# Performance work log

Measured on AMD Instinct MI355X. Metric: run time of the kernel, lower is better.

## Reference

```python
import jax, jax.numpy as jnp
import numpy as np

B, T, TREF, C, H = 2, 2048, 512, 768, 12
D = C // H


def setup_inputs() -> dict:
    key = jax.random.key(0)
    ks = jax.random.split(key, 20)
    s = 0.02  # init scale for weights
    inp = {
        "x": jax.random.normal(ks[0], (B, T, C), dtype=jnp.float32),
        "mask": jax.random.randint(ks[1], (B, 1, T, T), 0, 2, dtype=jnp.int32),
        "rel_pos": jax.random.normal(ks[2], (H, T, T), dtype=jnp.float32) * 0.1,
        "ref_feat": jax.random.normal(ks[3], (B, TREF, C), dtype=jnp.float32),
    }
    names = ["Wq", "Wk", "Wv", "Wrk", "Wrv", "Wo"]
    for i, n in enumerate(names):
        inp[n] = jax.random.normal(ks[4 + i], (C, C), dtype=jnp.float32) * s
        inp["b" + n[1:]] = jnp.zeros((C,), dtype=jnp.float32)
    return inp


def _heads(t, W, b):
    # nn.Linear: y = t @ W.T + b, then (B, L, H, D) -> (B, H, L, D)
    Bt, L, _ = t.shape
    return (t @ W.T + b).reshape(Bt, L, H, D).transpose(0, 2, 1, 3)


def reference(x, mask, rel_pos, ref_feat, Wq, bq, Wk, bk, Wv, bv,
              Wrk, brk, Wrv, brv, Wo, bo):
    Bx, Tx, Cx = x.shape
    Tref = ref_feat.shape[1]
    q = _heads(x, Wq, bq)                  # (B,H,T,D)
    k = _heads(x, Wk, bk)
    v = _heads(x, Wv, bv)
    rk = _heads(ref_feat, Wrk, brk)        # (B,H,Tref,D)
    rv = _heads(ref_feat, Wrv, brv)
    k = jnp.concatenate([k, rk], axis=2)   # (B,H,T+Tref,D)
    v = jnp.concatenate([v, rv], axis=2)
    # additive bias: -inf where mask==1 (self keys), rel_pos on self keys,
    # ref keys get 0 bias (mask padded with 0)
    bias_self = jnp.where(mask == 1, -jnp.inf, 0.0).astype(x.dtype) + rel_pos[None]  # (B,H,T,T)
    bias = jnp.pad(bias_self, ((0, 0), (0, 0), (0, 0), (0, Tref)))  # (B,H,T,T+Tref)
    scale = 1.0 / jnp.sqrt(jnp.asarray(D, dtype=x.dtype))
    scores = jnp.einsum('bhqd,bhkd->bhqk', q, k) * scale + bias
    attn = jax.nn.softmax(scores, axis=-1)
    y = jnp.einsum('bhqk,bhkd->bhqd', attn, v)
    y = y.transpose(0, 2, 1, 3).reshape(Bx, Tx, Cx)
    return y @ Wo.T + bo
```

## Files before the change

### kernel.cpp

```cpp
#include <hip/hip_runtime.h>


typedef __bf16 bf16x8 __attribute__((ext_vector_type(8)));
typedef float floatx4 __attribute__((ext_vector_type(4)));
typedef uint uintx2 __attribute__((ext_vector_type(2)));

__device__ __forceinline__ ushort f2bf(float f) {
  uint u = __builtin_bit_cast(uint, f);
  return (ushort)((u + 0x7FFFu + ((u >> 16) & 1u)) >> 16);
}

__device__ __forceinline__ uint pack2bf(float lo, float hi) {
  ushort a = __builtin_bit_cast(ushort, (__bf16)lo);
  ushort b = __builtin_bit_cast(ushort, (__bf16)hi);
  return (uint)a | ((uint)b << 16);
}

__device__ __forceinline__ float fexp2(float x) {
#if __has_builtin(__builtin_amdgcn_exp2f)
  return __builtin_amdgcn_exp2f(x);
#else
  return exp2f(x);
#endif
}

__device__ __forceinline__ void gld16(ushort* lds, const ushort* g) {
  __builtin_amdgcn_global_load_lds(
      (const __attribute__((address_space(1))) unsigned int*)g,
      (__attribute__((address_space(3))) unsigned int*)lds, 16, 0, 0);
}

__global__ __launch_bounds__(256) void cast_all(
    const float* __restrict__ x, const float* __restrict__ rf,
    const float* __restrict__ w0, const float* __restrict__ w1,
    const float* __restrict__ w2, const float* __restrict__ w3,
    const float* __restrict__ w4, const float* __restrict__ w5,
    ushort* __restrict__ dst) {
  size_t i4 = ((size_t)blockIdx.x * 256 + threadIdx.x) * 4;
  const float* src;
  size_t off;
  if (i4 < 3145728) { src = x; off = i4; }
  else if (i4 < 3932160) { src = rf; off = i4 - 3145728; }
  else {
    size_t r = i4 - 3932160;
    if (r < 589824) { src = w0; off = r; }
    else if (r < 2 * 589824) { src = w1; off = r - 589824; }
    else if (r < 3 * 589824) { src = w2; off = r - 2 * 589824; }
    else if (r < 4 * 589824) { src = w3; off = r - 3 * 589824; }
    else if (r < 5 * 589824) { src = w4; off = r - 4 * 589824; }
    else { src = w5; off = r - 5 * 589824; }
  }
  float4 v = *(const float4*)(src + off);
  ushort4 o;
  o.x = f2bf(v.x); o.y = f2bf(v.y); o.z = f2bf(v.z); o.w = f2bf(v.w);
  *(ushort4*)(dst + i4) = o;
}

__global__ __launch_bounds__(256) void pack_mask(
    const int* __restrict__ mask, unsigned long long* __restrict__ bits) {
  const int gid = blockIdx.x * 256 + threadIdx.x;
  const int4* src = (const int4*)(mask + (size_t)gid * 64);
  unsigned long long v = 0;
#pragma unroll
  for (int j = 0; j < 16; ++j) {
    int4 m = src[j];
    unsigned long long nib = (m.x ? 1ull : 0ull) | (m.y ? 2ull : 0ull) |
                             (m.z ? 4ull : 0ull) | (m.w ? 8ull : 0ull);
    v |= nib << (j * 4);
  }
  bits[gid] = v;
}

__device__ __forceinline__ void gemm_core(
    const ushort* __restrict__ Ab, const ushort* __restrict__ Bb,
    ushort* As, ushort* Bs, int tid, int quad, int l16, int mw, int nw,
    floatx4 acc[4][4]) {
  const int w = tid >> 6;
  const int r0 = tid >> 2, kp = (tid & 3) * 8;
  const size_t ga0 = (size_t)r0 * 768 + kp;
  const size_t ga1 = ga0 + (size_t)64 * 768;
#define GEMM_ISSUE(kb, p)                                   \
  do {                                                      \
    const int k0_ = (kb) * 32;                              \
    gld16(&As[(p) * 4096 + w * 512], Ab + ga0 + k0_);       \
    gld16(&As[(p) * 4096 + w * 512 + 2048], Ab + ga1 + k0_);\
    gld16(&Bs[(p) * 4096 + w * 512], Bb + ga0 + k0_);       \
    gld16(&Bs[(p) * 4096 + w * 512 + 2048], Bb + ga1 + k0_);\
  } while (0)
  GEMM_ISSUE(0, 0);
#pragma unroll 1
  for (int kb = 0; kb < 24; ++kb) {
    __syncthreads();
    if (kb < 23) GEMM_ISSUE(kb + 1, (kb + 1) & 1);
    const int p = kb & 1;
    bf16x8 af[4], bfr[4];
#pragma unroll
    for (int mt = 0; mt < 4; ++mt)
      af[mt] = *(const bf16x8*)&As[p * 4096 + (mw + mt * 16 + l16) * 32 + quad * 8];
#pragma unroll
    for (int nt = 0; nt < 4; ++nt)
      bfr[nt] = *(const bf16x8*)&Bs[p * 4096 + (nw + nt * 16 + l16) * 32 + quad * 8];
#pragma unroll
    for (int mt = 0; mt < 4; ++mt)
#pragma unroll
      for (int nt = 0; nt < 4; ++nt)
        acc[mt][nt] = __builtin_amdgcn_mfma_f32_16x16x32_bf16(af[mt], bfr[nt], acc[mt][nt], 0, 0, 0);
  }
#undef GEMM_ISSUE
}

template <int REF>
__global__ __launch_bounds__(256) void gemm_fused(
    const ushort* __restrict__ A, const ushort* __restrict__ W,
    const float* __restrict__ bA, const float* __restrict__ bB,
    const float* __restrict__ bC,
    ushort* __restrict__ oA, ushort* __restrict__ oB, ushort* __restrict__ oC) {
  const int bm = blockIdx.x, bn = blockIdx.y;
  const int tid = threadIdx.x;
  const int w = tid >> 6, lane = tid & 63, quad = lane >> 4, l16 = lane & 15;
  const int mw = (w >> 1) * 64, nw = (w & 1) * 64;

  __shared__ __align__(16) ushort As[2 * 4096];
  __shared__ __align__(16) ushort Bs[2 * 4096];

  floatx4 acc[4][4];
#pragma unroll
  for (int mt = 0; mt < 4; ++mt)
#pragma unroll
    for (int nt = 0; nt < 4; ++nt) acc[mt][nt] = (floatx4){0.f, 0.f, 0.f, 0.f};

  gemm_core(A + (size_t)bm * 128 * 768, W + (size_t)bn * 128 * 768,
            As, Bs, tid, quad, l16, mw, nw, acc);

  const int sec = bn / 6;
  const float* bp = sec == 0 ? bA : sec == 1 ? bB : bC;
  ushort* op = sec == 0 ? oA : sec == 1 ? oB : oC;
  const bool qlay = (REF == 0 && sec == 0);
  const bool vlay = (REF == 0) ? (sec == 2) : (sec == 1);
  const float scl = qlay ? 0.18033688011112042f : 1.0f;
#pragma unroll
  for (int nt = 0; nt < 4; ++nt) {
    const int nloc = (bn - sec * 6) * 128 + nw + nt * 16 + l16;
    const float bv = bp[nloc];
    const int hh = nloc >> 6, dd = nloc & 63;
    if (vlay) {
#pragma unroll
      for (int mt = 0; mt < 4; ++mt) {
        const int m0 = bm * 128 + mw + mt * 16 + quad * 4;
        int bb, t0;
        if (REF == 0) { bb = m0 >> 11; t0 = m0 & 2047; }
        else { bb = m0 >> 9; t0 = (m0 & 511) + 2048; }
        ushort4 o;
        o.x = f2bf(acc[mt][nt][0] + bv);
        o.y = f2bf(acc[mt][nt][1] + bv);
        o.z = f2bf(acc[mt][nt][2] + bv);
        o.w = f2bf(acc[mt][nt][3] + bv);
        *(ushort4*)&op[((size_t)(bb * 12 + hh) * 64 + dd) * 2560 + t0] = o;
      }
    } else {
#pragma unroll
      for (int mt = 0; mt < 4; ++mt)
#pragma unroll
        for (int i = 0; i < 4; ++i) {
          const int m = bm * 128 + mw + mt * 16 + quad * 4 + i;
          int bb, tt;
          if (REF == 0) { bb = m >> 11; tt = m & 2047; }
          else { bb = m >> 9; tt = (m & 511) + 2048; }
          const size_t idx = qlay ? (((size_t)(bb * 12 + hh) * 2048 + tt) * 64 + dd)
                                  : (((size_t)(bb * 12 + hh) * 2560 + tt) * 64 + dd);
          op[idx] = f2bf((acc[mt][nt][i] + bv) * scl);
        }
    }
  }
}

__global__ __launch_bounds__(256) void gemm_out(
    const ushort* __restrict__ A, const ushort* __restrict__ W,
    const float* __restrict__ bias, float* __restrict__ out) {
  const int bm = blockIdx.x, bn = blockIdx.y;
  const int tid = threadIdx.x;
  const int w = tid >> 6, lane = tid & 63, quad = lane >> 4, l16 = lane & 15;
  const int mw = (w >> 1) * 64, nw = (w & 1) * 64;

  __shared__ __align__(16) ushort As[2 * 4096];
  __shared__ __align__(16) ushort Bs[2 * 4096];

  floatx4 acc[4][4];
#pragma unroll
  for (int mt = 0; mt < 4; ++mt)
#pragma unroll
    for (int nt = 0; nt < 4; ++nt) acc[mt][nt] = (floatx4){0.f, 0.f, 0.f, 0.f};

  gemm_core(A + (size_t)bm * 128 * 768, W + (size_t)bn * 128 * 768,
            As, Bs, tid, quad, l16, mw, nw, acc);

#pragma unroll
  for (int nt = 0; nt < 4; ++nt) {
    const int n = bn * 128 + nw + nt * 16 + l16;
    const float bv = bias[n];
#pragma unroll
    for (int mt = 0; mt < 4; ++mt)
#pragma unroll
      for (int i = 0; i < 4; ++i) {
        const int m = bm * 128 + mw + mt * 16 + quad * 4 + i;
        out[(size_t)m * 768 + n] = acc[mt][nt][i] + bv;
      }
  }
}

__global__ __launch_bounds__(256, 3) void attn(
    const ushort* __restrict__ qb, const ushort* __restrict__ kb,
    const ushort* __restrict__ vb, const unsigned long long* __restrict__ bits,
    const float* __restrict__ relp, ushort* __restrict__ yb) {
  const int b = blockIdx.x, qt = blockIdx.y, h = blockIdx.z;
  const int tid = threadIdx.x;
  const int w = tid >> 6, lane = tid & 63, quad = lane >> 4, l16 = lane & 15;

  __shared__ __align__(16) ushort Kl[2][4096];
  __shared__ __align__(16) ushort Vtl[2][4096];
  __shared__ __align__(16) ushort Ps[4][8][16][8];

  const ushort* qsrc = qb + ((size_t)(b * 12 + h) * 2048 + qt * 64) * 64;
  const ushort* ksrc = kb + (size_t)(b * 12 + h) * 2560 * 64;
  const ushort* vtsrc = vb + (size_t)(b * 12 + h) * 64 * 2560;
  const int qrow = qt * 64 + w * 16 + l16;
  const unsigned long long* brow = bits + ((size_t)b * 2048 + qrow) * 32;
  const float* rrow = relp + ((size_t)h * 2048 + qrow) * 2048;

  const int krow = lane >> 3;
  const int kchunk = (lane & 7) ^ krow;

#pragma unroll
  for (int c = 0; c < 2; ++c) {
    const int rb = w * 16 + c * 8;
    gld16(&Kl[0][rb * 64], ksrc + (rb + krow) * 64 + kchunk * 8);
    gld16(&Vtl[0][rb * 64], vtsrc + (size_t)(rb + krow) * 2560 + kchunk * 8);
  }

  bf16x8 bQ[2];
  bQ[0] = *(const bf16x8*)(qsrc + (w * 16 + l16) * 64 + quad * 8);
  bQ[1] = *(const bf16x8*)(qsrc + (w * 16 + l16) * 64 + 32 + quad * 8);

  float4 rd[4];
#pragma unroll
  for (int mt = 0; mt < 4; ++mt)
    rd[mt] = *(const float4*)(rrow + mt * 16 + quad * 4);
  unsigned long long bnext = brow[0];

  floatx4 acc[4];
#pragma unroll
  for (int mt = 0; mt < 4; ++mt) acc[mt] = (floatx4){0.f, 0.f, 0.f, 0.f};
  float m_run = -__builtin_inff(), l_run = 0.f;

#pragma unroll 1
  for (int it = 0; it < 40; ++it) {
    const int p = it & 1;
    const bool self = it < 32;
    const unsigned long long bcur = bnext;
    __syncthreads();

    const int itn = it + 1;
    if (itn < 40) {
      const int pn = itn & 1;
#pragma unroll
      for (int c = 0; c < 2; ++c) {
        const int rb = w * 16 + c * 8;
        gld16(&Kl[pn][rb * 64],
              ksrc + (size_t)itn * 4096 + (rb + krow) * 64 + kchunk * 8);
        gld16(&Vtl[pn][rb * 64],
              vtsrc + (size_t)(rb + krow) * 2560 + itn * 64 + kchunk * 8);
      }
    }

    floatx4 st[4];
#pragma unroll
    for (int mt = 0; mt < 4; ++mt) st[mt] = (floatx4){0.f, 0.f, 0.f, 0.f};
#pragma unroll
    for (int kk = 0; kk < 2; ++kk)
#pragma unroll
      for (int mt = 0; mt < 4; ++mt) {
        const bf16x8 aK = *(const bf16x8*)
            &Kl[p][(mt * 16 + l16) * 64 + (((kk * 4 + quad) ^ (l16 & 7)) * 8)];
        st[mt] = __builtin_amdgcn_mfma_f32_16x16x32_bf16(aK, bQ[kk], st[mt], 0, 0, 0);
      }

    if (self) {
#pragma unroll
      for (int mt = 0; mt < 4; ++mt) {
        const float rr[4] = {rd[mt].x, rd[mt].y, rd[mt].z, rd[mt].w};
        const uint ni = (uint)(bcur >> (mt * 16 + quad * 4)) & 0xFu;
#pragma unroll
        for (int i = 0; i < 4; ++i) {
          const float sv = fmaf(rr[i], 1.4426950408889634f, st[mt][i]);
          st[mt][i] = (ni & (1u << i)) ? -__builtin_inff() : sv;
        }
      }
    }
    if (itn < 32) {
#pragma unroll
      for (int mt = 0; mt < 4; ++mt)
        rd[mt] = *(const float4*)(rrow + itn * 64 + mt * 16 + quad * 4);
      bnext = brow[itn];
    }

    float tm = fmaxf(fmaxf(st[0][0], st[0][1]), fmaxf(st[0][2], st[0][3]));
#pragma unroll
    for (int mt = 1; mt < 4; ++mt)
      tm = fmaxf(tm, fmaxf(fmaxf(st[mt][0], st[mt][1]), fmaxf(st[mt][2], st[mt][3])));
    tm = fmaxf(tm, __shfl_xor(tm, 16));
    tm = fmaxf(tm, __shfl_xor(tm, 32));
    float mref;
    if (__all(tm - m_run <= 8.f)) {
      mref = m_run;
    } else {
      const float mnew = fmaxf(m_run, tm);
      mref = (mnew == -__builtin_inff()) ? 0.f : mnew;
      const float alpha =
          (m_run == -__builtin_inff()) ? 0.f : fexp2(m_run - mnew);
      m_run = mnew;
      l_run *= alpha;
#pragma unroll
      for (int mt = 0; mt < 4; ++mt) acc[mt] *= alpha;
    }
    float rs = 0.f;
#pragma unroll
    for (int mt = 0; mt < 4; ++mt)
#pragma unroll
      for (int i = 0; i < 4; ++i) {
        const float pv = fexp2(st[mt][i] - mref);
        st[mt][i] = pv;
        rs += pv;
      }
    rs += __shfl_xor(rs, 16);
    rs += __shfl_xor(rs, 32);
    l_run += rs;

    {
      ushort* pwb = &Ps[w][quad >> 1][l16][(quad & 1) * 4];
#pragma unroll
      for (int mt = 0; mt < 4; ++mt) {
        uintx2 pkv;
        pkv.x = pack2bf(st[mt][0], st[mt][1]);
        pkv.y = pack2bf(st[mt][2], st[mt][3]);
        *(uintx2*)(pwb + mt * 256) = pkv;
      }
    }

    const bf16x8 bP0 = *(const bf16x8*)&Ps[w][quad][l16][0];
    const bf16x8 bP1 = *(const bf16x8*)&Ps[w][4 + quad][l16][0];
#pragma unroll
    for (int kk = 0; kk < 2; ++kk) {
      const bf16x8 bPk = kk ? bP1 : bP0;
#pragma unroll
      for (int mt = 0; mt < 4; ++mt) {
        const bf16x8 aV = *(const bf16x8*)
            &Vtl[p][(mt * 16 + l16) * 64 + (((kk * 4 + quad) ^ (l16 & 7)) * 8)];
        acc[mt] = __builtin_amdgcn_mfma_f32_16x16x32_bf16(aV, bPk, acc[mt], 0, 0, 0);
      }
    }
  }

  const float inv = 1.f / l_run;
  ushort* yrow = yb + ((size_t)b * 2048 + qt * 64 + w * 16 + l16) * 768 + h * 64;
#pragma unroll
  for (int mt = 0; mt < 4; ++mt)
#pragma unroll
    for (int i = 0; i < 4; ++i)
      yrow[mt * 16 + quad * 4 + i] = f2bf(acc[mt][i] * inv);
}

extern "C" void kernel_launch(void* const* d_in, const int* in_sizes, int n_in,
                              void* d_out, int out_size, void* d_ws, size_t ws_size,
                              hipStream_t stream) {
  const float* x = (const float*)d_in[0];
  const int* mask = (const int*)d_in[1];
  const float* relp = (const float*)d_in[2];
  const float* ref = (const float*)d_in[3];
  const float* Wq = (const float*)d_in[4];
  const float* bq = (const float*)d_in[5];
  const float* Wk = (const float*)d_in[6];
  const float* bk = (const float*)d_in[7];
  const float* Wv = (const float*)d_in[8];
  const float* bv = (const float*)d_in[9];
  const float* Wrk = (const float*)d_in[10];
  const float* brk = (const float*)d_in[11];
  const float* Wrv = (const float*)d_in[12];
  const float* brv = (const float*)d_in[13];
  const float* Wo = (const float*)d_in[14];
  const float* bo = (const float*)d_in[15];

  ushort* xb = (ushort*)d_ws;
  ushort* refb = xb + 3145728;
  ushort* wb = refb + 786432;
  ushort* qbuf = wb + 6 * 589824;
  ushort* kbuf = qbuf + 3145728;
  ushort* vbuf = kbuf + 3932160;
  ushort* ybuf = vbuf + 3932160;
  unsigned long long* bitsbuf = (unsigned long long*)(ybuf + 3145728);

  cast_all<<<7296, 256, 0, stream>>>(x, ref, Wq, Wk, Wv, Wrk, Wrv, Wo, xb);
  pack_mask<<<512, 256, 0, stream>>>(mask, bitsbuf);

  gemm_fused<0><<<dim3(32, 18), 256, 0, stream>>>(
      xb, wb, bq, bk, bv, qbuf, kbuf, vbuf);
  gemm_fused<1><<<dim3(8, 12), 256, 0, stream>>>(
      refb, wb + (size_t)3 * 589824, brk, brv, nullptr, kbuf, vbuf, nullptr);

  attn<<<dim3(2, 32, 12), 256, 0, stream>>>(qbuf, kbuf, vbuf, bitsbuf, relp, ybuf);

  gemm_out<<<dim3(32, 6), 256, 0, stream>>>(
      ybuf, wb + (size_t)5 * 589824, bo, (float*)d_out);
}
```

Baseline: 488.6 us.

## Hand-schedule attention loop with partial vmcnt waits and rewrite mask packing via ballot

The attention loop's __syncthreads is replaced with an explicit partial s_waitcnt plus s_barrier, so the prefetched rel_pos and mask-bit global loads for the next tile can stay in flight across the barrier. Those prefetches are issued before the QK MFMAs, sched_barriers pin the instruction order, and s_setprio raises wave priority around the MFMA blocks. Separately, pack_mask now builds each 64-bit mask word with a wave ballot over coalesced int loads, using twice as many blocks. The hard-coded vmcnt(5) depends on the exact count of outstanding loads, so a compiler scheduling change could make it wait on the wrong loads and read stale data.

New measurement: 510.7 us. 4.5% more time.

```diff
diff --git a/kernel.cpp b/kernel.cpp
--- a/kernel.cpp
+++ b/kernel.cpp
@@ -58,17 +58,16 @@
 
 __global__ __launch_bounds__(256) void pack_mask(
     const int* __restrict__ mask, unsigned long long* __restrict__ bits) {
-  const int gid = blockIdx.x * 256 + threadIdx.x;
-  const int4* src = (const int4*)(mask + (size_t)gid * 64);
-  unsigned long long v = 0;
-#pragma unroll
-  for (int j = 0; j < 16; ++j) {
-    int4 m = src[j];
-    unsigned long long nib = (m.x ? 1ull : 0ull) | (m.y ? 2ull : 0ull) |
-                             (m.z ? 4ull : 0ull) | (m.w ? 8ull : 0ull);
-    v |= nib << (j * 4);
-  }
-  bits[gid] = v;
+  const int wid = (blockIdx.x * 256 + threadIdx.x) >> 6;
+  const int lane = threadIdx.x & 63;
+  const int base = wid * 32;
+#pragma unroll 4
+  for (int j = 0; j < 32; ++j) {
+    const int wrd = base + j;
+    const int m = mask[(size_t)wrd * 64 + lane];
+    const unsigned long long v = __ballot(m != 0);
+    if (lane == 0) bits[wrd] = v;
+  }
 }
 
 __device__ __forceinline__ void gemm_core(
@@ -236,16 +235,17 @@
     gld16(&Kl[0][rb * 64], ksrc + (rb + krow) * 64 + kchunk * 8);
     gld16(&Vtl[0][rb * 64], vtsrc + (size_t)(rb + krow) * 2560 + kchunk * 8);
   }
+  __builtin_amdgcn_sched_barrier(0);
 
   bf16x8 bQ[2];
   bQ[0] = *(const bf16x8*)(qsrc + (w * 16 + l16) * 64 + quad * 8);
   bQ[1] = *(const bf16x8*)(qsrc + (w * 16 + l16) * 64 + 32 + quad * 8);
 
-  float4 rd[4];
+  float4 rdc[4];
 #pragma unroll
   for (int mt = 0; mt < 4; ++mt)
-    rd[mt] = *(const float4*)(rrow + mt * 16 + quad * 4);
-  unsigned long long bnext = brow[0];
+    rdc[mt] = *(const float4*)(rrow + mt * 16 + quad * 4);
+  unsigned long long bc = brow[0];
 
   floatx4 acc[4];
 #pragma unroll
@@ -256,8 +256,12 @@
   for (int it = 0; it < 40; ++it) {
     const int p = it & 1;
     const bool self = it < 32;
-    const unsigned long long bcur = bnext;
-    __syncthreads();
+    __builtin_amdgcn_sched_barrier(0);
+    if (it < 32) asm volatile("s_waitcnt vmcnt(5)" ::: "memory");
+    else asm volatile("s_waitcnt vmcnt(0)" ::: "memory");
+    __builtin_amdgcn_sched_barrier(0);
+    __builtin_amdgcn_s_barrier();
+    __builtin_amdgcn_sched_barrier(0);
 
     const int itn = it + 1;
     if (itn < 40) {
@@ -271,10 +275,21 @@
               vtsrc + (size_t)(rb + krow) * 2560 + itn * 64 + kchunk * 8);
       }
     }
+    __builtin_amdgcn_sched_barrier(0);
+    float4 rdn[4];
+    unsigned long long bn = 0;
+    if (itn < 32) {
+#pragma unroll
+      for (int mt = 0; mt < 4; ++mt)
+        rdn[mt] = *(const float4*)(rrow + itn * 64 + mt * 16 + quad * 4);
+      bn = brow[itn];
+    }
+    __builtin_amdgcn_sched_barrier(0);
 
     floatx4 st[4];
 #pragma unroll
     for (int mt = 0; mt < 4; ++mt) st[mt] = (floatx4){0.f, 0.f, 0.f, 0.f};
+    __builtin_amdgcn_s_setprio(1);
 #pragma unroll
     for (int kk = 0; kk < 2; ++kk)
 #pragma unroll
@@ -283,24 +298,19 @@
             &Kl[p][(mt * 16 + l16) * 64 + (((kk * 4 + quad) ^ (l16 & 7)) * 8)];
         st[mt] = __builtin_amdgcn_mfma_f32_16x16x32_bf16(aK, bQ[kk], st[mt], 0, 0, 0);
       }
+    __builtin_amdgcn_s_setprio(0);
 
     if (self) {
 #pragma unroll
       for (int mt = 0; mt < 4; ++mt) {
-        const float rr[4] = {rd[mt].x, rd[mt].y, rd[mt].z, rd[mt].w};
-        const uint ni = (uint)(bcur >> (mt * 16 + quad * 4)) & 0xFu;
+        const float rr[4] = {rdc[mt].x, rdc[mt].y, rdc[mt].z, rdc[mt].w};
+        const uint ni = (uint)(bc >> (mt * 16 + quad * 4)) & 0xFu;
 #pragma unroll
         for (int i = 0; i < 4; ++i) {
           const float sv = fmaf(rr[i], 1.4426950408889634f, st[mt][i]);
           st[mt][i] = (ni & (1u << i)) ? -__builtin_inff() : sv;
         }
       }
-    }
-    if (itn < 32) {
-#pragma unroll
-      for (int mt = 0; mt < 4; ++mt)
-        rd[mt] = *(const float4*)(rrow + itn * 64 + mt * 16 + quad * 4);
-      bnext = brow[itn];
     }
 
     float tm = fmaxf(fmaxf(st[0][0], st[0][1]), fmaxf(st[0][2], st[0][3]));
@@ -348,6 +358,7 @@
 
     const bf16x8 bP0 = *(const bf16x8*)&Ps[w][quad][l16][0];
     const bf16x8 bP1 = *(const bf16x8*)&Ps[w][4 + quad][l16][0];
+    __builtin_amdgcn_s_setprio(1);
 #pragma unroll
     for (int kk = 0; kk < 2; ++kk) {
       const bf16x8 bPk = kk ? bP1 : bP0;
@@ -357,6 +368,13 @@
             &Vtl[p][(mt * 16 + l16) * 64 + (((kk * 4 + quad) ^ (l16 & 7)) * 8)];
         acc[mt] = __builtin_amdgcn_mfma_f32_16x16x32_bf16(aV, bPk, acc[mt], 0, 0, 0);
       }
+    }
+    __builtin_amdgcn_s_setprio(0);
+
+    if (itn < 32) {
+#pragma unroll
+      for (int mt = 0; mt < 4; ++mt) rdc[mt] = rdn[mt];
+      bc = bn;
     }
   }
 
@@ -399,7 +417,7 @@
   unsigned long long* bitsbuf = (unsigned long long*)(ybuf + 3145728);
 
   cast_all<<<7296, 256, 0, stream>>>(x, ref, Wq, Wk, Wv, Wrk, Wrv, Wo, xb);
-  pack_mask<<<512, 256, 0, stream>>>(mask, bitsbuf);
+  pack_mask<<<1024, 256, 0, stream>>>(mask, bitsbuf);
 
   gemm_fused<0><<<dim3(32, 18), 256, 0, stream>>>(
       xb, wb, bq, bk, bv, qbuf, kbuf, vbuf);
```

## Split each attention key tile across two wave groups and merge partial softmax states

Applied to the files above, without the earlier changes.

The attention block grows from 4 to 8 waves. Each pair of waves shares a 16-row query slice, and each wave of the pair handles half of every 64-key tile. At the end, the two partial (m, l, acc) states are merged through shared memory before the output is written. The goal is more waves in flight per CU to hide global loads of rel_pos and the mask bits. The cost is an extra end-of-kernel reduction, two more barriers, and each wave keeping its own running max and sum.

Result: no change. 491.5 us (+0.6%).

```diff
diff --git a/kernel.cpp b/kernel.cpp
--- a/kernel.cpp
+++ b/kernel.cpp
@@ -208,43 +208,40 @@
   }
 }
 
-__global__ __launch_bounds__(256, 3) void attn(
+__global__ __launch_bounds__(512, 6) void attn(
     const ushort* __restrict__ qb, const ushort* __restrict__ kb,
     const ushort* __restrict__ vb, const unsigned long long* __restrict__ bits,
     const float* __restrict__ relp, ushort* __restrict__ yb) {
   const int b = blockIdx.x, qt = blockIdx.y, h = blockIdx.z;
   const int tid = threadIdx.x;
   const int w = tid >> 6, lane = tid & 63, quad = lane >> 4, l16 = lane & 15;
+  const int wl = w & 3, kh = w >> 2;
 
   __shared__ __align__(16) ushort Kl[2][4096];
   __shared__ __align__(16) ushort Vtl[2][4096];
-  __shared__ __align__(16) ushort Ps[4][8][16][8];
+  __shared__ __align__(16) ushort Ps[8][4][16][8];
 
   const ushort* qsrc = qb + ((size_t)(b * 12 + h) * 2048 + qt * 64) * 64;
   const ushort* ksrc = kb + (size_t)(b * 12 + h) * 2560 * 64;
   const ushort* vtsrc = vb + (size_t)(b * 12 + h) * 64 * 2560;
-  const int qrow = qt * 64 + w * 16 + l16;
+  const int qrow = qt * 64 + wl * 16 + l16;
   const unsigned long long* brow = bits + ((size_t)b * 2048 + qrow) * 32;
   const float* rrow = relp + ((size_t)h * 2048 + qrow) * 2048;
 
   const int krow = lane >> 3;
   const int kchunk = (lane & 7) ^ krow;
 
-#pragma unroll
-  for (int c = 0; c < 2; ++c) {
-    const int rb = w * 16 + c * 8;
-    gld16(&Kl[0][rb * 64], ksrc + (rb + krow) * 64 + kchunk * 8);
-    gld16(&Vtl[0][rb * 64], vtsrc + (size_t)(rb + krow) * 2560 + kchunk * 8);
-  }
+  gld16(&Kl[0][w * 512], ksrc + (w * 8 + krow) * 64 + kchunk * 8);
+  gld16(&Vtl[0][w * 512], vtsrc + (size_t)(w * 8 + krow) * 2560 + kchunk * 8);
 
   bf16x8 bQ[2];
-  bQ[0] = *(const bf16x8*)(qsrc + (w * 16 + l16) * 64 + quad * 8);
-  bQ[1] = *(const bf16x8*)(qsrc + (w * 16 + l16) * 64 + 32 + quad * 8);
-
-  float4 rd[4];
-#pragma unroll
-  for (int mt = 0; mt < 4; ++mt)
-    rd[mt] = *(const float4*)(rrow + mt * 16 + quad * 4);
+  bQ[0] = *(const bf16x8*)(qsrc + (wl * 16 + l16) * 64 + quad * 8);
+  bQ[1] = *(const bf16x8*)(qsrc + (wl * 16 + l16) * 64 + 32 + quad * 8);
+
+  float4 rd[2];
+#pragma unroll
+  for (int mt2 = 0; mt2 < 2; ++mt2)
+    rd[mt2] = *(const float4*)(rrow + kh * 32 + mt2 * 16 + quad * 4);
   unsigned long long bnext = brow[0];
 
   floatx4 acc[4];
@@ -262,51 +259,45 @@
     const int itn = it + 1;
     if (itn < 40) {
       const int pn = itn & 1;
-#pragma unroll
-      for (int c = 0; c < 2; ++c) {
-        const int rb = w * 16 + c * 8;
-        gld16(&Kl[pn][rb * 64],
-              ksrc + (size_t)itn * 4096 + (rb + krow) * 64 + kchunk * 8);
-        gld16(&Vtl[pn][rb * 64],
-              vtsrc + (size_t)(rb + krow) * 2560 + itn * 64 + kchunk * 8);
-      }
-    }
-
-    floatx4 st[4];
-#pragma unroll
-    for (int mt = 0; mt < 4; ++mt) st[mt] = (floatx4){0.f, 0.f, 0.f, 0.f};
+      gld16(&Kl[pn][w * 512],
+            ksrc + (size_t)itn * 4096 + (w * 8 + krow) * 64 + kchunk * 8);
+      gld16(&Vtl[pn][w * 512],
+            vtsrc + (size_t)(w * 8 + krow) * 2560 + itn * 64 + kchunk * 8);
+    }
+
+    floatx4 st[2];
+#pragma unroll
+    for (int mt2 = 0; mt2 < 2; ++mt2) st[mt2] = (floatx4){0.f, 0.f, 0.f, 0.f};
 #pragma unroll
     for (int kk = 0; kk < 2; ++kk)
 #pragma unroll
-      for (int mt = 0; mt < 4; ++mt) {
+      for (int mt2 = 0; mt2 < 2; ++mt2) {
         const bf16x8 aK = *(const bf16x8*)
-            &Kl[p][(mt * 16 + l16) * 64 + (((kk * 4 + quad) ^ (l16 & 7)) * 8)];
-        st[mt] = __builtin_amdgcn_mfma_f32_16x16x32_bf16(aK, bQ[kk], st[mt], 0, 0, 0);
+            &Kl[p][(kh * 32 + mt2 * 16 + l16) * 64 + (((kk * 4 + quad) ^ (l16 & 7)) * 8)];
+        st[mt2] = __builtin_amdgcn_mfma_f32_16x16x32_bf16(aK, bQ[kk], st[mt2], 0, 0, 0);
       }
 
     if (self) {
 #pragma unroll
-      for (int mt = 0; mt < 4; ++mt) {
-        const float rr[4] = {rd[mt].x, rd[mt].y, rd[mt].z, rd[mt].w};
-        const uint ni = (uint)(bcur >> (mt * 16 + quad * 4)) & 0xFu;
+      for (int mt2 = 0; mt2 < 2; ++mt2) {
+        const float rr[4] = {rd[mt2].x, rd[mt2].y, rd[mt2].z, rd[mt2].w};
+        const uint ni = (uint)(bcur >> (kh * 32 + mt2 * 16 + quad * 4)) & 0xFu;
 #pragma unroll
         for (int i = 0; i < 4; ++i) {
-          const float sv = fmaf(rr[i], 1.4426950408889634f, st[mt][i]);
-          st[mt][i] = (ni & (1u << i)) ? -__builtin_inff() : sv;
+          const float sv = fmaf(rr[i], 1.4426950408889634f, st[mt2][i]);
+          st[mt2][i] = (ni & (1u << i)) ? -__builtin_inff() : sv;
         }
       }
     }
     if (itn < 32) {
 #pragma unroll
-      for (int mt = 0; mt < 4; ++mt)
-        rd[mt] = *(const float4*)(rrow + itn * 64 + mt * 16 + quad * 4);
+      for (int mt2 = 0; mt2 < 2; ++mt2)
+        rd[mt2] = *(const float4*)(rrow + itn * 64 + kh * 32 + mt2 * 16 + quad * 4);
       bnext = brow[itn];
     }
 
     float tm = fmaxf(fmaxf(st[0][0], st[0][1]), fmaxf(st[0][2], st[0][3]));
-#pragma unroll
-    for (int mt = 1; mt < 4; ++mt)
-      tm = fmaxf(tm, fmaxf(fmaxf(st[mt][0], st[mt][1]), fmaxf(st[mt][2], st[mt][3])));
+    tm = fmaxf(tm, fmaxf(fmaxf(st[1][0], st[1][1]), fmaxf(st[1][2], st[1][3])));
     tm = fmaxf(tm, __shfl_xor(tm, 16));
     tm = fmaxf(tm, __shfl_xor(tm, 32));
     float mref;
@@ -324,11 +315,11 @@
     }
     float rs = 0.f;
 #pragma unroll
-    for (int mt = 0; mt < 4; ++mt)
+    for (int mt2 = 0; mt2 < 2; ++mt2)
 #pragma unroll
       for (int i = 0; i < 4; ++i) {
-        const float pv = fexp2(st[mt][i] - mref);
-        st[mt][i] = pv;
+        const float pv = fexp2(st[mt2][i] - mref);
+        st[mt2][i] = pv;
         rs += pv;
       }
     rs += __shfl_xor(rs, 16);
@@ -338,35 +329,50 @@
     {
       ushort* pwb = &Ps[w][quad >> 1][l16][(quad & 1) * 4];
 #pragma unroll
-      for (int mt = 0; mt < 4; ++mt) {
+      for (int mt2 = 0; mt2 < 2; ++mt2) {
         uintx2 pkv;
-        pkv.x = pack2bf(st[mt][0], st[mt][1]);
-        pkv.y = pack2bf(st[mt][2], st[mt][3]);
-        *(uintx2*)(pwb + mt * 256) = pkv;
-      }
-    }
-
-    const bf16x8 bP0 = *(const bf16x8*)&Ps[w][quad][l16][0];
-    const bf16x8 bP1 = *(const bf16x8*)&Ps[w][4 + quad][l16][0];
-#pragma unroll
-    for (int kk = 0; kk < 2; ++kk) {
-      const bf16x8 bPk = kk ? bP1 : bP0;
-#pragma unroll
-      for (int mt = 0; mt < 4; ++mt) {
-        const bf16x8 aV = *(const bf16x8*)
-            &Vtl[p][(mt * 16 + l16) * 64 + (((kk * 4 + quad) ^ (l16 & 7)) * 8)];
-        acc[mt] = __builtin_amdgcn_mfma_f32_16x16x32_bf16(aV, bPk, acc[mt], 0, 0, 0);
-      }
-    }
-  }
-
-  const float inv = 1.f / l_run;
-  ushort* yrow = yb + ((size_t)b * 2048 + qt * 64 + w * 16 + l16) * 768 + h * 64;
-#pragma unroll
-  for (int mt = 0; mt < 4; ++mt)
-#pragma unroll
-    for (int i = 0; i < 4; ++i)
-      yrow[mt * 16 + quad * 4 + i] = f2bf(acc[mt][i] * inv);
+        pkv.x = pack2bf(st[mt2][0], st[mt2][1]);
+        pkv.y = pack2bf(st[mt2][2], st[mt2][3]);
+        *(uintx2*)(pwb + mt2 * 256) = pkv;
+      }
+    }
+
+    const bf16x8 bP = *(const bf16x8*)&Ps[w][quad][l16][0];
+#pragma unroll
+    for (int mt = 0; mt < 4; ++mt) {
+      const bf16x8 aV = *(const bf16x8*)
+          &Vtl[p][(mt * 16 + l16) * 64 + (((kh * 4 + quad) ^ (l16 & 7)) * 8)];
+      acc[mt] = __builtin_amdgcn_mfma_f32_16x16x32_bf16(aV, bP, acc[mt], 0, 0, 0);
+    }
+  }
+
+  __syncthreads();
+  floatx4* accbuf = (floatx4*)Kl;
+  float2* mlbuf = (float2*)Ps;
+  if (kh == 1) {
+    const int li = wl * 64 + lane;
+#pragma unroll
+    for (int mt = 0; mt < 4; ++mt) accbuf[li * 4 + mt] = acc[mt];
+    mlbuf[li] = (float2){m_run, l_run};
+  }
+  __syncthreads();
+  if (kh == 0) {
+    const int li = wl * 64 + lane;
+    const float2 ml1 = mlbuf[li];
+    const float M = fmaxf(m_run, ml1.x);
+    const float a0 = fexp2(m_run - M), a1 = fexp2(ml1.x - M);
+    const float l = l_run * a0 + ml1.y * a1;
+    const float inv = 1.f / l;
+    ushort* yrow = yb + ((size_t)b * 2048 + qt * 64 + wl * 16 + l16) * 768 + h * 64;
+#pragma unroll
+    for (int mt = 0; mt < 4; ++mt) {
+      const floatx4 o1 = accbuf[li * 4 + mt];
+#pragma unroll
+      for (int i = 0; i < 4; ++i)
+        yrow[mt * 16 + quad * 4 + i] =
+            f2bf((acc[mt][i] * a0 + o1[i] * a1) * inv);
+    }
+  }
 }
 
 extern "C" void kernel_launch(void* const* d_in, const int* in_sizes, int n_in,
@@ -406,7 +412,7 @@
   gemm_fused<1><<<dim3(8, 12), 256, 0, stream>>>(
       refb, wb + (size_t)3 * 589824, brk, brv, nullptr, kbuf, vbuf, nullptr);
 
-  attn<<<dim3(2, 32, 12), 256, 0, stream>>>(qbuf, kbuf, vbuf, bitsbuf, relp, ybuf);
+  attn<<<dim3(2, 32, 12), 512, 0, stream>>>(qbuf, kbuf, vbuf, bitsbuf, relp, ybuf);
 
   gemm_out<<<dim3(32, 6), 256, 0, stream>>>(
       ybuf, wb + (size_t)5 * 589824, bo, (float*)d_out);
```
